# Optimization experiments

Measured on AMD Instinct MI355X. Metric: run time of the kernel, lower is better.

Reference implementation:

```python
import jax, jax.numpy as jnp
import numpy as np

N = 100000      # nodes
E = 3200000     # edges (avg degree 32)
F_IN = 128      # input features
HID = 16        # hidden channels (hardcoded in Net)
C = 8           # num_classes


def setup_inputs() -> dict:
    key = jax.random.key(0)
    ks = jax.random.split(key, 6)
    x = jax.random.normal(ks[0], (N, F_IN), dtype=jnp.float32)
    edge_index = jax.random.randint(ks[1], (2, E), 0, N, dtype=jnp.int32)
    W1 = jax.random.normal(ks[2], (F_IN, HID), dtype=jnp.float32) / np.sqrt(F_IN)
    b1 = jnp.zeros((HID,), dtype=jnp.float32)
    W2 = jax.random.normal(ks[3], (HID, C), dtype=jnp.float32) / np.sqrt(HID)
    b2 = jnp.zeros((C,), dtype=jnp.float32)
    return {"x": x, "edge_index": edge_index, "W1": W1, "b1": b1, "W2": W2, "b2": b2}


def _gcn_conv(h, W, b, src, dst, norm):
    # GCNConv: x' = D^{-1/2} (A + I) D^{-1/2} (x W) + b
    h = h @ W                                  # [N, out] transform first (small out dim)
    msg = h[src] * norm[:, None]               # gather + edge normalization  [E+N, out]
    agg = jax.ops.segment_sum(msg, dst, num_segments=N)  # scatter-add to targets
    return agg + b


def reference(x, edge_index, W1, b1, W2, b2):
    row, col = edge_index[0], edge_index[1]
    loop = jnp.arange(N, dtype=row.dtype)
    src = jnp.concatenate([row, loop])         # add self-loops
    dst = jnp.concatenate([col, loop])
    # symmetric normalization: deg over aggregation targets (incl. self-loops)
    deg = jax.ops.segment_sum(jnp.ones_like(dst, dtype=jnp.float32), dst, num_segments=N)
    dinv = jnp.where(deg > 0, jax.lax.rsqrt(deg), 0.0)
    norm = dinv[src] * dinv[dst]               # [E+N]

    h = jax.nn.relu(_gcn_conv(x, W1, b1, src, dst, norm))
    # F.dropout with training=False is the identity (inference reference)
    out = _gcn_conv(h, W2, b2, src, dst, norm)
    return jax.nn.log_softmax(out, axis=1)
```

## Files before the change

### kernel.cpp

```cpp
#include <hip/hip_runtime.h>

#define NN 100000
#define EE 3200000
#define FIN 128
#define HID 16
#define NC 8

#define CHUNK 12500
#define NBLK 256
#define BW 256
#define NBUK ((NN + BW - 1) / BW)
#define EPT 13
#define CAP 9216
#define BEPT 9

__device__ __forceinline__ unsigned bf16pair(float a, float b) {
    unsigned ua = __float_as_uint(a), ub = __float_as_uint(b);
    ua = ua + 0x7fffu + ((ua >> 16) & 1u);
    ub = ub + 0x7fffu + ((ub >> 16) & 1u);
    return (ua >> 16) | (ub & 0xffff0000u);
}

__global__ __launch_bounds__(512) void k_zero_cursor(unsigned* __restrict__ cursor) {
    int t = threadIdx.x;
    if (t < NBUK) cursor[t] = 0u;
}

__global__ __launch_bounds__(1024) void k_binscatter(const int* __restrict__ row,
                                                     const int* __restrict__ col,
                                                     unsigned* __restrict__ cursor,
                                                     unsigned* __restrict__ bins_pk) {
    __shared__ unsigned s_cnt[NBUK];
    __shared__ unsigned s_start[NBUK];
    __shared__ unsigned s_off[NBUK];
    __shared__ unsigned s_gb[NBUK];
    __shared__ unsigned stg[CHUNK];
    __shared__ unsigned short bktid[CHUNK];
    int t = threadIdx.x;
    for (int i = t; i < NBUK; i += 1024) s_cnt[i] = 0u;
    __syncthreads();
    int base = blockIdx.x * CHUNK;
    unsigned val[EPT];
    unsigned short bk[EPT];
    #pragma unroll
    for (int k = 0; k < EPT; ++k) {
        int i = t + k * 1024;
        if (i < CHUNK) {
            int s = row[base + i];
            int d = col[base + i];
            unsigned b = (unsigned)d >> 8;
            val[k] = (unsigned)s | ((unsigned)(d & 255) << 17);
            bk[k] = (unsigned short)b;
            atomicAdd(&s_cnt[b], 1u);
        }
    }
    __syncthreads();
    for (int i = t; i < NBUK; i += 1024)
        s_gb[i] = atomicAdd(&cursor[i], s_cnt[i]);
    __syncthreads();
    for (int off = 1; off < NBUK; off <<= 1) {
        unsigned v = 0u;
        if (t < NBUK && t >= off) v = s_cnt[t - off];
        __syncthreads();
        if (t < NBUK) s_cnt[t] += v;
        __syncthreads();
    }
    if (t < NBUK) {
        unsigned st = (t == 0) ? 0u : s_cnt[t - 1];
        s_start[t] = st;
        s_off[t] = st;
    }
    __syncthreads();
    #pragma unroll
    for (int k = 0; k < EPT; ++k) {
        int i = t + k * 1024;
        if (i < CHUNK) {
            unsigned b = bk[k];
            unsigned r = atomicAdd(&s_off[b], 1u);
            stg[r] = val[k];
            bktid[r] = (unsigned short)b;
        }
    }
    __syncthreads();
    for (int i = t; i < CHUNK; i += 1024) {
        unsigned b = bktid[i];
        bins_pk[(size_t)b * CAP + s_gb[b] + ((unsigned)i - s_start[b])] = stg[i];
    }
}

__global__ __launch_bounds__(1024) void k_build(const unsigned* __restrict__ bins_pk,
                                                const unsigned* __restrict__ cursor,
                                                uint2* __restrict__ row_se,
                                                float* __restrict__ dinv,
                                                unsigned* __restrict__ srcsort) {
    __shared__ unsigned cnt[BW];
    __shared__ unsigned offn[BW];
    __shared__ unsigned stg[CAP];
    int t = threadIdx.x, b = blockIdx.x;
    if (t < BW) cnt[t] = 0u;
    __syncthreads();
    unsigned m = cursor[b];
    unsigned base = (unsigned)b * CAP;
    unsigned val[BEPT];
    unsigned char dl[BEPT];
    #pragma unroll
    for (int k = 0; k < BEPT; ++k) {
        unsigned i = t + k * 1024u;
        if (i < m) {
            unsigned w = bins_pk[base + i];
            val[k] = w & 0x1FFFFu;
            dl[k] = (unsigned char)(w >> 17);
            atomicAdd(&cnt[dl[k]], 1u);
        }
    }
    __syncthreads();
    for (int off = 1; off < BW; off <<= 1) {
        unsigned v = 0u;
        if (t < BW && t >= off) v = cnt[t - off];
        __syncthreads();
        if (t < BW) cnt[t] += v;
        __syncthreads();
    }
    if (t < BW) {
        unsigned st = (t == 0) ? 0u : cnt[t - 1];
        offn[t] = st;
        int node = b * BW + t;
        if (node < NN) {
            row_se[node] = uint2{base + st, base + cnt[t]};
            dinv[node] = rsqrtf(1.0f + (float)(cnt[t] - st));
        }
    }
    __syncthreads();
    #pragma unroll
    for (int k = 0; k < BEPT; ++k) {
        unsigned i = t + k * 1024u;
        if (i < m) {
            unsigned r = atomicAdd(&offn[dl[k]], 1u);
            stg[r] = val[k];
        }
    }
    __syncthreads();
    for (unsigned i = t; i < m; i += 1024u)
        srcsort[base + i] = stg[i];
}

__global__ __launch_bounds__(256) void k_gemm1(const float* __restrict__ x,
                                               const float* __restrict__ W1,
                                               const float* __restrict__ dinv,
                                               unsigned* __restrict__ hs1b) {
    __shared__ float w1s[FIN * HID];
    __shared__ float xs[64 * 132];
    int t = threadIdx.x;
    int r0 = blockIdx.x * 64;
    for (int i = t; i < FIN * HID; i += 256) w1s[i] = W1[i];
    int maxr = NN - r0; if (maxr > 64) maxr = 64;
    const float4* x4 = reinterpret_cast<const float4*>(x + (size_t)r0 * FIN);
    #pragma unroll
    for (int i = 0; i < 8; ++i) {
        int fi = t + i * 256;
        int f = fi * 4;
        int r = f >> 7, k = f & 127;
        if (r < maxr) {
            float4 v = x4[fi];
            *reinterpret_cast<float4*>(&xs[r * 132 + k]) = v;
        }
    }
    __syncthreads();
    int r = t >> 2;
    int cg = (t & 3) * 4;
    if (r < maxr) {
        float4 acc = {0.f, 0.f, 0.f, 0.f};
        const float* xr = &xs[r * 132];
        #pragma unroll 4
        for (int k = 0; k < FIN; ++k) {
            float xv = xr[k];
            const float4 w = *reinterpret_cast<const float4*>(&w1s[k * HID + cg]);
            acc.x += xv * w.x; acc.y += xv * w.y; acc.z += xv * w.z; acc.w += xv * w.w;
        }
        int rr = r0 + r;
        float di = dinv[rr];
        uint2 pk;
        pk.x = bf16pair(acc.x * di, acc.y * di);
        pk.y = bf16pair(acc.z * di, acc.w * di);
        *reinterpret_cast<uint2*>(&hs1b[(rr << 3) + (cg >> 1)]) = pk;
    }
}

__global__ __launch_bounds__(256) void k_l1(const uint2* __restrict__ row_se,
                                            const unsigned* __restrict__ srcsort,
                                            const unsigned* __restrict__ hs1b,
                                            const float* __restrict__ dinv,
                                            const float* __restrict__ W2,
                                            const float* __restrict__ b1,
                                            unsigned* __restrict__ hs2b) {
    __shared__ float htile[32 * 17];
    __shared__ float w2s[HID * NC];
    int t = threadIdx.x;
    if (t < HID * NC) w2s[t] = W2[t];
    int g = t >> 3;
    int c2 = t & 7;
    int n = blockIdx.x * 32 + g;
    uint2 se = row_se[n];
    unsigned e = se.x, e1 = se.y;
    float a0 = 0.f, a1 = 0.f;
    for (; e + 3 < e1; e += 4) {
        int s0 = srcsort[e];
        int s1 = srcsort[e + 1];
        int s2 = srcsort[e + 2];
        int s3 = srcsort[e + 3];
        unsigned v0 = hs1b[(s0 << 3) + c2];
        unsigned v1 = hs1b[(s1 << 3) + c2];
        unsigned v2 = hs1b[(s2 << 3) + c2];
        unsigned v3 = hs1b[(s3 << 3) + c2];
        a0 += __uint_as_float(v0 << 16) + __uint_as_float(v1 << 16)
            + __uint_as_float(v2 << 16) + __uint_as_float(v3 << 16);
        a1 += __uint_as_float(v0 & 0xffff0000u) + __uint_as_float(v1 & 0xffff0000u)
            + __uint_as_float(v2 & 0xffff0000u) + __uint_as_float(v3 & 0xffff0000u);
    }
    for (; e < e1; ++e) {
        unsigned v = hs1b[((int)srcsort[e] << 3) + c2];
        a0 += __uint_as_float(v << 16);
        a1 += __uint_as_float(v & 0xffff0000u);
    }
    {
        unsigned v = hs1b[(n << 3) + c2];
        a0 += __uint_as_float(v << 16);
        a1 += __uint_as_float(v & 0xffff0000u);
    }
    float di = dinv[n];
    int c = c2 * 2;
    htile[g * 17 + c]     = fmaxf(a0 * di + b1[c], 0.f);
    htile[g * 17 + c + 1] = fmaxf(a1 * di + b1[c + 1], 0.f);
    __syncthreads();
    if (t < 128) {
        int n2 = t >> 2, j2 = t & 3;
        const float* hr = &htile[n2 * 17];
        float oa = 0.f, ob = 0.f;
        #pragma unroll
        for (int k = 0; k < HID; ++k) {
            float hv = hr[k];
            oa += hv * w2s[k * NC + 2 * j2];
            ob += hv * w2s[k * NC + 2 * j2 + 1];
        }
        int node2 = blockIdx.x * 32 + n2;
        float d2 = dinv[node2];
        hs2b[(node2 << 2) + j2] = bf16pair(oa * d2, ob * d2);
    }
}

__global__ __launch_bounds__(256) void k_l2(const uint2* __restrict__ row_se,
                                            const unsigned* __restrict__ srcsort,
                                            const unsigned* __restrict__ hs2b,
                                            const float* __restrict__ dinv,
                                            const float* __restrict__ b2,
                                            float* __restrict__ out) {
    int t = threadIdx.x;
    int g = t >> 2;
    int c2 = t & 3;
    int n = blockIdx.x * 64 + g;
    if (n >= NN) return;
    uint2 se = row_se[n];
    unsigned e = se.x, e1 = se.y;
    float a0 = 0.f, a1 = 0.f;
    for (; e + 3 < e1; e += 4) {
        int s0 = srcsort[e];
        int s1 = srcsort[e + 1];
        int s2 = srcsort[e + 2];
        int s3 = srcsort[e + 3];
        unsigned v0 = hs2b[(s0 << 2) + c2];
        unsigned v1 = hs2b[(s1 << 2) + c2];
        unsigned v2 = hs2b[(s2 << 2) + c2];
        unsigned v3 = hs2b[(s3 << 2) + c2];
        a0 += __uint_as_float(v0 << 16) + __uint_as_float(v1 << 16)
            + __uint_as_float(v2 << 16) + __uint_as_float(v3 << 16);
        a1 += __uint_as_float(v0 & 0xffff0000u) + __uint_as_float(v1 & 0xffff0000u)
            + __uint_as_float(v2 & 0xffff0000u) + __uint_as_float(v3 & 0xffff0000u);
    }
    for (; e < e1; ++e) {
        unsigned v = hs2b[((int)srcsort[e] << 2) + c2];
        a0 += __uint_as_float(v << 16);
        a1 += __uint_as_float(v & 0xffff0000u);
    }
    {
        unsigned v = hs2b[(n << 2) + c2];
        a0 += __uint_as_float(v << 16);
        a1 += __uint_as_float(v & 0xffff0000u);
    }
    float di = dinv[n];
    int c = c2 * 2;
    float v0 = a0 * di + b2[c];
    float v1 = a1 * di + b2[c + 1];
    float m = fmaxf(v0, v1);
    m = fmaxf(m, __shfl_xor(m, 1, 4));
    m = fmaxf(m, __shfl_xor(m, 2, 4));
    float s = expf(v0 - m) + expf(v1 - m);
    s += __shfl_xor(s, 1, 4);
    s += __shfl_xor(s, 2, 4);
    float ls = logf(s);
    float2 o = {v0 - m - ls, v1 - m - ls};
    *reinterpret_cast<float2*>(&out[(n << 3) + c]) = o;
}

extern "C" void kernel_launch(void* const* d_in, const int* in_sizes, int n_in,
                              void* d_out, int out_size, void* d_ws, size_t ws_size,
                              hipStream_t stream) {
    const float* x   = (const float*)d_in[0];
    const int*   ei  = (const int*)d_in[1];
    const float* W1  = (const float*)d_in[2];
    const float* b1  = (const float*)d_in[3];
    const float* W2  = (const float*)d_in[4];
    const float* b2  = (const float*)d_in[5];
    float* out = (float*)d_out;

    const int* row = ei;
    const int* col = ei + EE;

    float*    ws      = (float*)d_ws;
    float*    dinv    = ws;
    unsigned* hs1b    = (unsigned*)(dinv + NN);
    unsigned* hs2b    = hs1b + (size_t)NN * 8;
    uint2*    row_se  = (uint2*)(hs2b + (size_t)NN * 4);
    unsigned* cursor  = (unsigned*)(row_se + NN);
    unsigned* bins_pk = cursor + NBUK;
    unsigned* srcsort = bins_pk + (size_t)NBUK * CAP;

    k_zero_cursor <<<1, 512, 0, stream>>>(cursor);
    k_binscatter  <<<NBLK, 1024, 0, stream>>>(row, col, cursor, bins_pk);
    k_build       <<<NBUK, 1024, 0, stream>>>(bins_pk, cursor, row_se, dinv, srcsort);
    k_gemm1       <<<(NN + 63) / 64, 256, 0, stream>>>(x, W1, dinv, hs1b);
    k_l1          <<<NN / 32, 256, 0, stream>>>(row_se, srcsort, hs1b, dinv, W2, b1, hs2b);
    k_l2          <<<(NN + 63) / 64, 256, 0, stream>>>(row_se, srcsort, hs2b, dinv, b2, out);
}
```

Measured before the change: 112.1 us.

## Widen gather loads to uint2, halve binscatter chunk, write bins per bucket

The layer-1 and layer-2 aggregation kernels now have each thread gather 8-byte uint2 values holding four bf16 channels instead of 4-byte pairs. This halves threads per node, packs more nodes per block and leaves fewer shuffles in the log-softmax. The binscatter kernel uses twice as many blocks with half-sized chunks, and drops the per-entry bucket-id array by having each wavefront copy whole bucket segments out. These changes target memory-transaction count and occupancy, but per-bucket write loops may become unbalanced because bucket sizes vary.

```diff
diff --git a/kernel.cpp b/kernel.cpp
--- a/kernel.cpp
+++ b/kernel.cpp
@@ -6,11 +6,11 @@
 #define HID 16
 #define NC 8
 
-#define CHUNK 12500
-#define NBLK 256
+#define CHUNK 6250
+#define NBLK 512
 #define BW 256
 #define NBUK ((NN + BW - 1) / BW)
-#define EPT 13
+#define EPT 7
 #define CAP 9216
 #define BEPT 9
 
@@ -20,6 +20,8 @@
     ub = ub + 0x7fffu + ((ub >> 16) & 1u);
     return (ua >> 16) | (ub & 0xffff0000u);
 }
+__device__ __forceinline__ float bflo(unsigned v) { return __uint_as_float(v << 16); }
+__device__ __forceinline__ float bfhi(unsigned v) { return __uint_as_float(v & 0xffff0000u); }
 
 __global__ __launch_bounds__(512) void k_zero_cursor(unsigned* __restrict__ cursor) {
     int t = threadIdx.x;
@@ -35,7 +37,6 @@
     __shared__ unsigned s_off[NBUK];
     __shared__ unsigned s_gb[NBUK];
     __shared__ unsigned stg[CHUNK];
-    __shared__ unsigned short bktid[CHUNK];
     int t = threadIdx.x;
     for (int i = t; i < NBUK; i += 1024) s_cnt[i] = 0u;
     __syncthreads();
@@ -78,13 +79,16 @@
             unsigned b = bk[k];
             unsigned r = atomicAdd(&s_off[b], 1u);
             stg[r] = val[k];
-            bktid[r] = (unsigned short)b;
-        }
-    }
-    __syncthreads();
-    for (int i = t; i < CHUNK; i += 1024) {
-        unsigned b = bktid[i];
-        bins_pk[(size_t)b * CAP + s_gb[b] + ((unsigned)i - s_start[b])] = stg[i];
+        }
+    }
+    __syncthreads();
+    int w = t >> 6, lane = t & 63;
+    for (int b = w; b < NBUK; b += 16) {
+        unsigned st = s_start[b];
+        unsigned en = s_cnt[b];
+        unsigned dst = (unsigned)b * CAP + s_gb[b];
+        for (unsigned i = st + lane; i < en; i += 64)
+            bins_pk[dst + (i - st)] = stg[i];
     }
 }
 
@@ -188,117 +192,119 @@
 
 __global__ __launch_bounds__(256) void k_l1(const uint2* __restrict__ row_se,
                                             const unsigned* __restrict__ srcsort,
-                                            const unsigned* __restrict__ hs1b,
+                                            const uint2* __restrict__ hs1b2,
                                             const float* __restrict__ dinv,
                                             const float* __restrict__ W2,
                                             const float* __restrict__ b1,
                                             unsigned* __restrict__ hs2b) {
-    __shared__ float htile[32 * 17];
+    __shared__ float htile[64 * 17];
     __shared__ float w2s[HID * NC];
     int t = threadIdx.x;
     if (t < HID * NC) w2s[t] = W2[t];
-    int g = t >> 3;
-    int c2 = t & 7;
-    int n = blockIdx.x * 32 + g;
+    int g = t >> 2;
+    int c4 = t & 3;
+    int n = blockIdx.x * 64 + g;
+    if (n < NN) {
+        uint2 se = row_se[n];
+        unsigned e = se.x, e1 = se.y;
+        float a0 = 0.f, a1 = 0.f, a2 = 0.f, a3 = 0.f;
+        for (; e + 3 < e1; e += 4) {
+            int s0 = srcsort[e];
+            int s1 = srcsort[e + 1];
+            int s2 = srcsort[e + 2];
+            int s3 = srcsort[e + 3];
+            uint2 v0 = hs1b2[(s0 << 2) + c4];
+            uint2 v1 = hs1b2[(s1 << 2) + c4];
+            uint2 v2 = hs1b2[(s2 << 2) + c4];
+            uint2 v3 = hs1b2[(s3 << 2) + c4];
+            a0 += bflo(v0.x) + bflo(v1.x) + bflo(v2.x) + bflo(v3.x);
+            a1 += bfhi(v0.x) + bfhi(v1.x) + bfhi(v2.x) + bfhi(v3.x);
+            a2 += bflo(v0.y) + bflo(v1.y) + bflo(v2.y) + bflo(v3.y);
+            a3 += bfhi(v0.y) + bfhi(v1.y) + bfhi(v2.y) + bfhi(v3.y);
+        }
+        for (; e < e1; ++e) {
+            uint2 v = hs1b2[((int)srcsort[e] << 2) + c4];
+            a0 += bflo(v.x); a1 += bfhi(v.x); a2 += bflo(v.y); a3 += bfhi(v.y);
+        }
+        {
+            uint2 v = hs1b2[(n << 2) + c4];
+            a0 += bflo(v.x); a1 += bfhi(v.x); a2 += bflo(v.y); a3 += bfhi(v.y);
+        }
+        float di = dinv[n];
+        int c = c4 * 4;
+        htile[g * 17 + c]     = fmaxf(a0 * di + b1[c], 0.f);
+        htile[g * 17 + c + 1] = fmaxf(a1 * di + b1[c + 1], 0.f);
+        htile[g * 17 + c + 2] = fmaxf(a2 * di + b1[c + 2], 0.f);
+        htile[g * 17 + c + 3] = fmaxf(a3 * di + b1[c + 3], 0.f);
+    }
+    __syncthreads();
+    {
+        int n2 = t >> 2, j2 = t & 3;
+        int node2 = blockIdx.x * 64 + n2;
+        if (node2 < NN) {
+            const float* hr = &htile[n2 * 17];
+            float oa = 0.f, ob = 0.f;
+            #pragma unroll
+            for (int k = 0; k < HID; ++k) {
+                float hv = hr[k];
+                oa += hv * w2s[k * NC + 2 * j2];
+                ob += hv * w2s[k * NC + 2 * j2 + 1];
+            }
+            float d2 = dinv[node2];
+            hs2b[(node2 << 2) + j2] = bf16pair(oa * d2, ob * d2);
+        }
+    }
+}
+
+__global__ __launch_bounds__(256) void k_l2(const uint2* __restrict__ row_se,
+                                            const unsigned* __restrict__ srcsort,
+                                            const uint2* __restrict__ hs2b2,
+                                            const float* __restrict__ dinv,
+                                            const float* __restrict__ b2,
+                                            float* __restrict__ out) {
+    int t = threadIdx.x;
+    int g = t >> 1;
+    int p = t & 1;
+    int n = blockIdx.x * 128 + g;
+    if (n >= NN) return;
     uint2 se = row_se[n];
     unsigned e = se.x, e1 = se.y;
-    float a0 = 0.f, a1 = 0.f;
+    float a0 = 0.f, a1 = 0.f, a2 = 0.f, a3 = 0.f;
     for (; e + 3 < e1; e += 4) {
         int s0 = srcsort[e];
         int s1 = srcsort[e + 1];
         int s2 = srcsort[e + 2];
         int s3 = srcsort[e + 3];
-        unsigned v0 = hs1b[(s0 << 3) + c2];
-        unsigned v1 = hs1b[(s1 << 3) + c2];
-        unsigned v2 = hs1b[(s2 << 3) + c2];
-        unsigned v3 = hs1b[(s3 << 3) + c2];
-        a0 += __uint_as_float(v0 << 16) + __uint_as_float(v1 << 16)
-            + __uint_as_float(v2 << 16) + __uint_as_float(v3 << 16);
-        a1 += __uint_as_float(v0 & 0xffff0000u) + __uint_as_float(v1 & 0xffff0000u)
-            + __uint_as_float(v2 & 0xffff0000u) + __uint_as_float(v3 & 0xffff0000u);
+        uint2 v0 = hs2b2[(s0 << 1) + p];
+        uint2 v1 = hs2b2[(s1 << 1) + p];
+        uint2 v2 = hs2b2[(s2 << 1) + p];
+        uint2 v3 = hs2b2[(s3 << 1) + p];
+        a0 += bflo(v0.x) + bflo(v1.x) + bflo(v2.x) + bflo(v3.x);
+        a1 += bfhi(v0.x) + bfhi(v1.x) + bfhi(v2.x) + bfhi(v3.x);
+        a2 += bflo(v0.y) + bflo(v1.y) + bflo(v2.y) + bflo(v3.y);
+        a3 += bfhi(v0.y) + bfhi(v1.y) + bfhi(v2.y) + bfhi(v3.y);
     }
     for (; e < e1; ++e) {
-        unsigned v = hs1b[((int)srcsort[e] << 3) + c2];
-        a0 += __uint_as_float(v << 16);
-        a1 += __uint_as_float(v & 0xffff0000u);
+        uint2 v = hs2b2[((int)srcsort[e] << 1) + p];
+        a0 += bflo(v.x); a1 += bfhi(v.x); a2 += bflo(v.y); a3 += bfhi(v.y);
     }
     {
-        unsigned v = hs1b[(n << 3) + c2];
-        a0 += __uint_as_float(v << 16);
-        a1 += __uint_as_float(v & 0xffff0000u);
+        uint2 v = hs2b2[(n << 1) + p];
+        a0 += bflo(v.x); a1 += bfhi(v.x); a2 += bflo(v.y); a3 += bfhi(v.y);
     }
     float di = dinv[n];
-    int c = c2 * 2;
-    htile[g * 17 + c]     = fmaxf(a0 * di + b1[c], 0.f);
-    htile[g * 17 + c + 1] = fmaxf(a1 * di + b1[c + 1], 0.f);
-    __syncthreads();
-    if (t < 128) {
-        int n2 = t >> 2, j2 = t & 3;
-        const float* hr = &htile[n2 * 17];
-        float oa = 0.f, ob = 0.f;
-        #pragma unroll
-        for (int k = 0; k < HID; ++k) {
-            float hv = hr[k];
-            oa += hv * w2s[k * NC + 2 * j2];
-            ob += hv * w2s[k * NC + 2 * j2 + 1];
-        }
-        int node2 = blockIdx.x * 32 + n2;
-        float d2 = dinv[node2];
-        hs2b[(node2 << 2) + j2] = bf16pair(oa * d2, ob * d2);
-    }
-}
-
-__global__ __launch_bounds__(256) void k_l2(const uint2* __restrict__ row_se,
-                                            const unsigned* __restrict__ srcsort,
-                                            const unsigned* __restrict__ hs2b,
-                                            const float* __restrict__ dinv,
-                                            const float* __restrict__ b2,
-                                            float* __restrict__ out) {
-    int t = threadIdx.x;
-    int g = t >> 2;
-    int c2 = t & 3;
-    int n = blockIdx.x * 64 + g;
-    if (n >= NN) return;
-    uint2 se = row_se[n];
-    unsigned e = se.x, e1 = se.y;
-    float a0 = 0.f, a1 = 0.f;
-    for (; e + 3 < e1; e += 4) {
-        int s0 = srcsort[e];
-        int s1 = srcsort[e + 1];
-        int s2 = srcsort[e + 2];
-        int s3 = srcsort[e + 3];
-        unsigned v0 = hs2b[(s0 << 2) + c2];
-        unsigned v1 = hs2b[(s1 << 2) + c2];
-        unsigned v2 = hs2b[(s2 << 2) + c2];
-        unsigned v3 = hs2b[(s3 << 2) + c2];
-        a0 += __uint_as_float(v0 << 16) + __uint_as_float(v1 << 16)
-            + __uint_as_float(v2 << 16) + __uint_as_float(v3 << 16);
-        a1 += __uint_as_float(v0 & 0xffff0000u) + __uint_as_float(v1 & 0xffff0000u)
-            + __uint_as_float(v2 & 0xffff0000u) + __uint_as_float(v3 & 0xffff0000u);
-    }
-    for (; e < e1; ++e) {
-        unsigned v = hs2b[((int)srcsort[e] << 2) + c2];
-        a0 += __uint_as_float(v << 16);
-        a1 += __uint_as_float(v & 0xffff0000u);
-    }
-    {
-        unsigned v = hs2b[(n << 2) + c2];
-        a0 += __uint_as_float(v << 16);
-        a1 += __uint_as_float(v & 0xffff0000u);
-    }
-    float di = dinv[n];
-    int c = c2 * 2;
+    int c = p * 4;
     float v0 = a0 * di + b2[c];
     float v1 = a1 * di + b2[c + 1];
-    float m = fmaxf(v0, v1);
-    m = fmaxf(m, __shfl_xor(m, 1, 4));
-    m = fmaxf(m, __shfl_xor(m, 2, 4));
-    float s = expf(v0 - m) + expf(v1 - m);
-    s += __shfl_xor(s, 1, 4);
-    s += __shfl_xor(s, 2, 4);
+    float v2 = a2 * di + b2[c + 2];
+    float v3 = a3 * di + b2[c + 3];
+    float m = fmaxf(fmaxf(v0, v1), fmaxf(v2, v3));
+    m = fmaxf(m, __shfl_xor(m, 1, 2));
+    float s = expf(v0 - m) + expf(v1 - m) + expf(v2 - m) + expf(v3 - m);
+    s += __shfl_xor(s, 1, 2);
     float ls = logf(s);
-    float2 o = {v0 - m - ls, v1 - m - ls};
-    *reinterpret_cast<float2*>(&out[(n << 3) + c]) = o;
+    float4 o = {v0 - m - ls, v1 - m - ls, v2 - m - ls, v3 - m - ls};
+    *reinterpret_cast<float4*>(&out[(n << 3) + c]) = o;
 }
 
 extern "C" void kernel_launch(void* const* d_in, const int* in_sizes, int n_in,
@@ -328,6 +334,6 @@
     k_binscatter  <<<NBLK, 1024, 0, stream>>>(row, col, cursor, bins_pk);
     k_build       <<<NBUK, 1024, 0, stream>>>(bins_pk, cursor, row_se, dinv, srcsort);
     k_gemm1       <<<(NN + 63) / 64, 256, 0, stream>>>(x, W1, dinv, hs1b);
-    k_l1          <<<NN / 32, 256, 0, stream>>>(row_se, srcsort, hs1b, dinv, W2, b1, hs2b);
-    k_l2          <<<(NN + 63) / 64, 256, 0, stream>>>(row_se, srcsort, hs2b, dinv, b2, out);
-}
+    k_l1          <<<(NN + 63) / 64, 256, 0, stream>>>(row_se, srcsort, (const uint2*)hs1b, dinv, W2, b1, hs2b);
+    k_l2          <<<(NN + 127) / 128, 256, 0, stream>>>(row_se, srcsort, (const uint2*)hs2b, dinv, b2, out);
+}
```

Measured after the change: 128.2 us. 1.14x slower.
